# Kernel tuning notes

Hardware: AMD Instinct MI355X
Metric: run time of the kernel (lower is better)

The kernel has to match this reference:

```python
import jax, jax.numpy as jnp
import numpy as np

HEADS = 8
DIM_HEAD = 32


def setup_inputs() -> dict:
    key = jax.random.key(0)
    k1, k2, k3, k4 = jax.random.split(key, 4)
    dim, hidden = 256, HEADS * DIM_HEAD
    x = jax.random.normal(k1, (4, dim, 48, 48), dtype=jnp.float32)
    # 1x1 conv weights stored as [out_ch, in_ch]
    w_qkv = jax.random.normal(k2, (3 * hidden, dim), dtype=jnp.float32) * (dim ** -0.5)
    w_out = jax.random.normal(k3, (dim, hidden), dtype=jnp.float32) * (hidden ** -0.5)
    b_out = jax.random.normal(k4, (dim,), dtype=jnp.float32) * 0.01
    return {"x": x, "w_qkv": w_qkv, "w_out": w_out, "b_out": b_out}


def reference(x, w_qkv, w_out, b_out):
    B, C, H, W = x.shape
    n = H * W
    scale = DIM_HEAD ** -0.5
    # 1x1 conv QKV projection: [B, 3*hidden, H, W] -> [B, 3, heads, dh, n]
    qkv = jnp.einsum('oc,bchw->bohw', w_qkv, x).reshape(B, 3, HEADS, DIM_HEAD, n)
    q, k, v = qkv[:, 0], qkv[:, 1], qkv[:, 2]  # each [B, h, dh, n]
    sim = jnp.einsum('bhdi,bhdj->bhij', q, k) * scale  # [B, h, n, n]
    attn = jax.nn.softmax(sim, axis=-1)
    out = jnp.einsum('bhij,bhdj->bhdi', attn, v)  # [B, h, dh, n] -> channels (h d)
    out = out.reshape(B, HEADS * DIM_HEAD, H, W)
    return jnp.einsum('oc,bchw->bohw', w_out, out) + b_out[None, :, None, None]
```

## Files before the change

### kernel.cpp

```cpp
#include <hip/hip_runtime.h>
#include <hip/hip_bf16.h>

#define NSP 2304
#define NB  4

typedef unsigned short u16;
typedef __attribute__((ext_vector_type(8))) short short8;
typedef __attribute__((ext_vector_type(4))) short short4v;
typedef __attribute__((ext_vector_type(4))) float f32x4;
typedef __attribute__((ext_vector_type(4))) unsigned short u16x4;

#define K1S 0.25508040852656425f

static __device__ inline u16 f2bf(float f) {
  return __builtin_bit_cast(unsigned short, __float2bfloat16(f));
}

__global__ __launch_bounds__(256) void convert_w(
    const float* __restrict__ wq, const float* __restrict__ wo,
    u16* __restrict__ dst) {
  int i = (blockIdx.x * 256 + threadIdx.x) * 4;
  float4 v;
  if (i < 196608) v = *(const float4*)(wq + i);
  else            v = *(const float4*)(wo + (i - 196608));
  u16x4 p = {f2bf(v.x), f2bf(v.y), f2bf(v.z), f2bf(v.w)};
  *(u16x4*)(dst + i) = p;
}

__global__ __launch_bounds__(256) void transpose_x(
    const float* __restrict__ x, u16* __restrict__ xT) {
  __shared__ float tile[32][33];
  const int t = threadIdx.x;
  const int n0 = blockIdx.x * 32, c0 = blockIdx.y * 32, b = blockIdx.z;
  const float* xb = x + ((size_t)b * 256 + c0) * NSP + n0;
#pragma unroll
  for (int e = t; e < 1024; e += 256) {
    int cc = e >> 5, nn = e & 31;
    tile[cc][nn] = xb[(size_t)cc * NSP + nn];
  }
  __syncthreads();
  u16* xTb = xT + ((size_t)b * NSP + n0) * 256 + c0;
#pragma unroll
  for (int e = t; e < 1024; e += 256) {
    int nn = e >> 5, cc = e & 31;
    xTb[(size_t)nn * 256 + cc] = f2bf(tile[cc][nn]);
  }
}

template <int EPI>
__global__ __launch_bounds__(256) void gemm_mfma(
    const u16* __restrict__ A, const u16* __restrict__ B,
    u16* __restrict__ qkT, u16* __restrict__ vbuf,
    float* __restrict__ outf, const float* __restrict__ bias, int N) {
  __shared__ u16 As[64][264];
  __shared__ u16 Bs[64][264];
  const int t = threadIdx.x, lane = t & 63, wid = t >> 6;
  const int lo = lane & 15, g = lane >> 4;
  const int wr = wid >> 1, wc = wid & 1;
  const int row0 = blockIdx.y * 64, col0 = blockIdx.x * 64, b = blockIdx.z;

  const int sr = t >> 2, c4 = t & 3;
  const u16* Arow = A + (size_t)(row0 + sr) * 256;
  const u16* Brow = B + ((size_t)b * N + col0 + sr) * 256;
#pragma unroll
  for (int i = 0; i < 8; ++i) {
    int col = (c4 + 4 * i) * 8;
    *(uint4*)&As[sr][col] = *(const uint4*)&Arow[col];
    *(uint4*)&Bs[sr][col] = *(const uint4*)&Brow[col];
  }
  __syncthreads();

  f32x4 acc[2][2];
#pragma unroll
  for (int i = 0; i < 2; ++i)
#pragma unroll
    for (int j = 0; j < 2; ++j) acc[i][j] = (f32x4){0, 0, 0, 0};

  const int ar0 = wr * 32 + lo, br0 = wc * 32 + lo;
#pragma unroll
  for (int kk = 0; kk < 8; ++kk) {
    int kc = kk * 32 + g * 8;
    short8 a0 = *(const short8*)&As[ar0][kc];
    short8 a1 = *(const short8*)&As[ar0 + 16][kc];
    short8 b0 = *(const short8*)&Bs[br0][kc];
    short8 b1 = *(const short8*)&Bs[br0 + 16][kc];
    acc[0][0] = __builtin_amdgcn_mfma_f32_16x16x32_bf16(a0, b0, acc[0][0], 0, 0, 0);
    acc[0][1] = __builtin_amdgcn_mfma_f32_16x16x32_bf16(a0, b1, acc[0][1], 0, 0, 0);
    acc[1][0] = __builtin_amdgcn_mfma_f32_16x16x32_bf16(a1, b0, acc[1][0], 0, 0, 0);
    acc[1][1] = __builtin_amdgcn_mfma_f32_16x16x32_bf16(a1, b1, acc[1][1], 0, 0, 0);
  }

  const float qs = (EPI == 0 && row0 < 256) ? K1S : 1.0f;
#pragma unroll
  for (int m2 = 0; m2 < 2; ++m2)
#pragma unroll
    for (int n2 = 0; n2 < 2; ++n2) {
      int m = row0 + wr * 32 + m2 * 16 + g * 4;
      int n = col0 + wc * 32 + n2 * 16 + lo;
      if constexpr (EPI == 0) {
        if (row0 < 512) {
          u16x4 pk = {f2bf(acc[m2][n2][0] * qs), f2bf(acc[m2][n2][1] * qs),
                      f2bf(acc[m2][n2][2] * qs), f2bf(acc[m2][n2][3] * qs)};
          *(u16x4*)(qkT + ((size_t)b * NSP + n) * 512 + m) = pk;
        } else {
#pragma unroll
          for (int r = 0; r < 4; ++r)
            vbuf[((size_t)b * 256 + (m - 512 + r)) * NSP + n] =
                f2bf(acc[m2][n2][r]);
        }
      } else {
#pragma unroll
        for (int r = 0; r < 4; ++r)
          outf[((size_t)b * 256 + m + r) * NSP + n] =
              acc[m2][n2][r] + bias[m + r];
      }
    }
}

__global__ __launch_bounds__(256) void attn_mfma(
    const u16* __restrict__ qkT, const u16* __restrict__ vbuf,
    u16* __restrict__ attnoT) {
  const int it = blockIdx.x, h = blockIdx.y, b = blockIdx.z;
  const int t = threadIdx.x, lane = t & 63, wq = t >> 6;
  const int lo = lane & 15, g = lane >> 4;
  const int i0 = it * 64;

  const u16* qkTb = qkT + (size_t)b * NSP * 512;
  const u16* vb   = vbuf + ((size_t)b * 256 + h * 32) * NSP;
  u16* ob = attnoT + ((size_t)b * NSP + i0) * 256 + h * 32;

  __shared__ u16 Kt[2][64][40];
  __shared__ u16 Vs[2][32][72];

  short8 qf = *(const short8*)(qkTb + (size_t)(i0 + wq * 16 + lo) * 512 +
                               h * 32 + g * 8);

  const int kr = t >> 2, kp = (t & 3) * 8;
  const int vr = t >> 3, vp = (t & 7) * 8;
  const u16* ksrc = qkTb + 256 + h * 32 + kp;
  const u16* vsrc = vb + (size_t)vr * NSP + vp;

  uint4 kreg = *(const uint4*)(ksrc + (size_t)kr * 512);
  uint4 vreg = *(const uint4*)(vsrc);
  *(uint4*)&Kt[0][kr][kp] = kreg;
  *(uint4*)&Vs[0][vr][vp] = vreg;
  __syncthreads();

  short8 ones;
#pragma unroll
  for (int e = 0; e < 8; ++e) ones[e] = (short)0x3F80;

  f32x4 acc0 = {0, 0, 0, 0}, acc1 = {0, 0, 0, 0}, accl = {0, 0, 0, 0};

  for (int s = 0; s < 36; ++s) {
    const int cur = s & 1;
    if (s + 1 < 36) {
      int j0n = (s + 1) * 64;
      kreg = *(const uint4*)(ksrc + (size_t)(j0n + kr) * 512);
      vreg = *(const uint4*)(vsrc + j0n);
    }

    f32x4 sv[4];
#pragma unroll
    for (int jt = 0; jt < 4; ++jt) {
      short8 kf = *(const short8*)&Kt[cur][jt * 16 + lo][g * 8];
      sv[jt] = __builtin_amdgcn_mfma_f32_16x16x32_bf16(
          kf, qf, (f32x4){0, 0, 0, 0}, 0, 0, 0);
    }

    short8 pf0, pf1;
#pragma unroll
    for (int e = 0; e < 8; ++e) {
      pf0[e] = (short)f2bf(__builtin_amdgcn_exp2f(sv[e >> 2][e & 3]));
      pf1[e] = (short)f2bf(__builtin_amdgcn_exp2f(sv[2 + (e >> 2)][e & 3]));
    }

    short4v v00a = *(const short4v*)&Vs[cur][lo][4 * g];
    short4v v00b = *(const short4v*)&Vs[cur][lo][16 + 4 * g];
    short4v v01a = *(const short4v*)&Vs[cur][lo][32 + 4 * g];
    short4v v01b = *(const short4v*)&Vs[cur][lo][48 + 4 * g];
    short4v v10a = *(const short4v*)&Vs[cur][16 + lo][4 * g];
    short4v v10b = *(const short4v*)&Vs[cur][16 + lo][16 + 4 * g];
    short4v v11a = *(const short4v*)&Vs[cur][16 + lo][32 + 4 * g];
    short4v v11b = *(const short4v*)&Vs[cur][16 + lo][48 + 4 * g];
    short8 vf00 = __builtin_shufflevector(v00a, v00b, 0, 1, 2, 3, 4, 5, 6, 7);
    short8 vf01 = __builtin_shufflevector(v01a, v01b, 0, 1, 2, 3, 4, 5, 6, 7);
    short8 vf10 = __builtin_shufflevector(v10a, v10b, 0, 1, 2, 3, 4, 5, 6, 7);
    short8 vf11 = __builtin_shufflevector(v11a, v11b, 0, 1, 2, 3, 4, 5, 6, 7);

    acc0 = __builtin_amdgcn_mfma_f32_16x16x32_bf16(pf0, vf00, acc0, 0, 0, 0);
    acc1 = __builtin_amdgcn_mfma_f32_16x16x32_bf16(pf0, vf10, acc1, 0, 0, 0);
    accl = __builtin_amdgcn_mfma_f32_16x16x32_bf16(pf0, ones, accl, 0, 0, 0);
    acc0 = __builtin_amdgcn_mfma_f32_16x16x32_bf16(pf1, vf01, acc0, 0, 0, 0);
    acc1 = __builtin_amdgcn_mfma_f32_16x16x32_bf16(pf1, vf11, acc1, 0, 0, 0);
    accl = __builtin_amdgcn_mfma_f32_16x16x32_bf16(pf1, ones, accl, 0, 0, 0);

    if (s + 1 < 36) {
      *(uint4*)&Kt[cur ^ 1][kr][kp] = kreg;
      *(uint4*)&Vs[cur ^ 1][vr][vp] = vreg;
    }
    __syncthreads();
  }

#pragma unroll
  for (int r = 0; r < 4; ++r) {
    float inv = 1.0f / accl[r];
    int row = wq * 16 + g * 4 + r;
    ob[(size_t)row * 256 + lo]      = f2bf(acc0[r] * inv);
    ob[(size_t)row * 256 + 16 + lo] = f2bf(acc1[r] * inv);
  }
}

extern "C" void kernel_launch(void* const* d_in, const int* in_sizes, int n_in,
                              void* d_out, int out_size, void* d_ws, size_t ws_size,
                              hipStream_t stream) {
  const float* x     = (const float*)d_in[0];
  const float* w_qkv = (const float*)d_in[1];
  const float* w_out = (const float*)d_in[2];
  const float* b_out = (const float*)d_in[3];
  float* out = (float*)d_out;

  u16* wbf    = (u16*)d_ws;
  u16* xT     = wbf + 262144;
  u16* qkT    = xT + (size_t)NB * NSP * 256;
  u16* vbuf   = qkT + (size_t)NB * NSP * 512;
  u16* attnoT = vbuf + (size_t)NB * 256 * NSP;

  dim3 blk(256);
  convert_w<<<256, blk, 0, stream>>>(w_qkv, w_out, wbf);
  transpose_x<<<dim3(NSP / 32, 8, NB), blk, 0, stream>>>(x, xT);
  gemm_mfma<0><<<dim3(NSP / 64, 12, NB), blk, 0, stream>>>(
      wbf, xT, qkT, vbuf, nullptr, nullptr, NSP);
  attn_mfma<<<dim3(NSP / 64, 8, NB), blk, 0, stream>>>(qkT, vbuf, attnoT);
  gemm_mfma<1><<<dim3(NSP / 64, 4, NB), blk, 0, stream>>>(
      wbf + 196608, attnoT, nullptr, nullptr, out, b_out, NSP);
}
```

Before: 81.51 us.

## Give each attention wave two query tiles and pack bf16 conversions

The attention kernel now runs 128 threads per block instead of 256, and each wave handles 32 query rows instead of 16. Each K and V fragment read from LDS is therefore reused for two query tiles, halving LDS traffic per MFMA. Each thread issues twice the global loads when staging K and V, and the V shared tile padding changes from 72 to 68. The exp results are packed to bf16 with the v_cvt_pk_bf16_f32 instruction, trading fewer waves per block and more registers for better data reuse.

```diff
diff --git a/kernel.cpp b/kernel.cpp
--- a/kernel.cpp
+++ b/kernel.cpp
@@ -14,6 +14,11 @@
 
 static __device__ inline u16 f2bf(float f) {
   return __builtin_bit_cast(unsigned short, __float2bfloat16(f));
+}
+static __device__ inline unsigned cvtpk(float a, float b) {
+  unsigned r;
+  asm("v_cvt_pk_bf16_f32 %0, %1, %2" : "=v"(r) : "v"(a), "v"(b));
+  return r;
 }
 
 __global__ __launch_bounds__(256) void convert_w(
@@ -117,11 +122,11 @@
     }
 }
 
-__global__ __launch_bounds__(256) void attn_mfma(
+__global__ __launch_bounds__(128) void attn_mfma(
     const u16* __restrict__ qkT, const u16* __restrict__ vbuf,
     u16* __restrict__ attnoT) {
   const int it = blockIdx.x, h = blockIdx.y, b = blockIdx.z;
-  const int t = threadIdx.x, lane = t & 63, wq = t >> 6;
+  const int t = threadIdx.x, lane = t & 63, w = t >> 6;
   const int lo = lane & 15, g = lane >> 4;
   const int i0 = it * 64;
 
@@ -130,51 +135,50 @@
   u16* ob = attnoT + ((size_t)b * NSP + i0) * 256 + h * 32;
 
   __shared__ u16 Kt[2][64][40];
-  __shared__ u16 Vs[2][32][72];
-
-  short8 qf = *(const short8*)(qkTb + (size_t)(i0 + wq * 16 + lo) * 512 +
-                               h * 32 + g * 8);
+  __shared__ u16 Vs[2][32][68];
+
+  short8 qfA = *(const short8*)(qkTb + (size_t)(i0 + w * 32 + lo) * 512 +
+                                h * 32 + g * 8);
+  short8 qfB = *(const short8*)(qkTb + (size_t)(i0 + w * 32 + 16 + lo) * 512 +
+                                h * 32 + g * 8);
 
   const int kr = t >> 2, kp = (t & 3) * 8;
   const int vr = t >> 3, vp = (t & 7) * 8;
-  const u16* ksrc = qkTb + 256 + h * 32 + kp;
-  const u16* vsrc = vb + (size_t)vr * NSP + vp;
-
-  uint4 kreg = *(const uint4*)(ksrc + (size_t)kr * 512);
-  uint4 vreg = *(const uint4*)(vsrc);
-  *(uint4*)&Kt[0][kr][kp] = kreg;
-  *(uint4*)&Vs[0][vr][vp] = vreg;
+  const u16* ksrc  = qkTb + 256 + h * 32 + kp;
+  const u16* vsrc0 = vb + (size_t)vr * NSP + vp;
+  const u16* vsrc1 = vb + (size_t)(vr + 16) * NSP + vp;
+
+  uint4 k0 = *(const uint4*)(ksrc + (size_t)kr * 512);
+  uint4 k1 = *(const uint4*)(ksrc + (size_t)(kr + 32) * 512);
+  uint4 v0 = *(const uint4*)(vsrc0);
+  uint4 v1 = *(const uint4*)(vsrc1);
+  *(uint4*)&Kt[0][kr][kp]      = k0;
+  *(uint4*)&Kt[0][kr + 32][kp] = k1;
+  *(uint4*)&Vs[0][vr][vp]      = v0;
+  *(uint4*)&Vs[0][vr + 16][vp] = v1;
   __syncthreads();
 
   short8 ones;
 #pragma unroll
   for (int e = 0; e < 8; ++e) ones[e] = (short)0x3F80;
 
-  f32x4 acc0 = {0, 0, 0, 0}, acc1 = {0, 0, 0, 0}, accl = {0, 0, 0, 0};
+  f32x4 a0A = {0, 0, 0, 0}, a1A = {0, 0, 0, 0}, alA = {0, 0, 0, 0};
+  f32x4 a0B = {0, 0, 0, 0}, a1B = {0, 0, 0, 0}, alB = {0, 0, 0, 0};
 
   for (int s = 0; s < 36; ++s) {
     const int cur = s & 1;
     if (s + 1 < 36) {
       int j0n = (s + 1) * 64;
-      kreg = *(const uint4*)(ksrc + (size_t)(j0n + kr) * 512);
-      vreg = *(const uint4*)(vsrc + j0n);
-    }
-
-    f32x4 sv[4];
-#pragma unroll
-    for (int jt = 0; jt < 4; ++jt) {
-      short8 kf = *(const short8*)&Kt[cur][jt * 16 + lo][g * 8];
-      sv[jt] = __builtin_amdgcn_mfma_f32_16x16x32_bf16(
-          kf, qf, (f32x4){0, 0, 0, 0}, 0, 0, 0);
-    }
-
-    short8 pf0, pf1;
-#pragma unroll
-    for (int e = 0; e < 8; ++e) {
-      pf0[e] = (short)f2bf(__builtin_amdgcn_exp2f(sv[e >> 2][e & 3]));
-      pf1[e] = (short)f2bf(__builtin_amdgcn_exp2f(sv[2 + (e >> 2)][e & 3]));
-    }
-
+      k0 = *(const uint4*)(ksrc + (size_t)(j0n + kr) * 512);
+      k1 = *(const uint4*)(ksrc + (size_t)(j0n + kr + 32) * 512);
+      v0 = *(const uint4*)(vsrc0 + j0n);
+      v1 = *(const uint4*)(vsrc1 + j0n);
+    }
+
+    short8 kf0 = *(const short8*)&Kt[cur][lo][g * 8];
+    short8 kf1 = *(const short8*)&Kt[cur][16 + lo][g * 8];
+    short8 kf2 = *(const short8*)&Kt[cur][32 + lo][g * 8];
+    short8 kf3 = *(const short8*)&Kt[cur][48 + lo][g * 8];
     short4v v00a = *(const short4v*)&Vs[cur][lo][4 * g];
     short4v v00b = *(const short4v*)&Vs[cur][lo][16 + 4 * g];
     short4v v01a = *(const short4v*)&Vs[cur][lo][32 + 4 * g];
@@ -188,26 +192,61 @@
     short8 vf10 = __builtin_shufflevector(v10a, v10b, 0, 1, 2, 3, 4, 5, 6, 7);
     short8 vf11 = __builtin_shufflevector(v11a, v11b, 0, 1, 2, 3, 4, 5, 6, 7);
 
-    acc0 = __builtin_amdgcn_mfma_f32_16x16x32_bf16(pf0, vf00, acc0, 0, 0, 0);
-    acc1 = __builtin_amdgcn_mfma_f32_16x16x32_bf16(pf0, vf10, acc1, 0, 0, 0);
-    accl = __builtin_amdgcn_mfma_f32_16x16x32_bf16(pf0, ones, accl, 0, 0, 0);
-    acc0 = __builtin_amdgcn_mfma_f32_16x16x32_bf16(pf1, vf01, acc0, 0, 0, 0);
-    acc1 = __builtin_amdgcn_mfma_f32_16x16x32_bf16(pf1, vf11, acc1, 0, 0, 0);
-    accl = __builtin_amdgcn_mfma_f32_16x16x32_bf16(pf1, ones, accl, 0, 0, 0);
+#pragma unroll
+    for (int qh = 0; qh < 2; ++qh) {
+      short8 qf = qh ? qfB : qfA;
+      f32x4 sv0 = __builtin_amdgcn_mfma_f32_16x16x32_bf16(kf0, qf, (f32x4){0,0,0,0}, 0, 0, 0);
+      f32x4 sv1 = __builtin_amdgcn_mfma_f32_16x16x32_bf16(kf1, qf, (f32x4){0,0,0,0}, 0, 0, 0);
+      f32x4 sv2 = __builtin_amdgcn_mfma_f32_16x16x32_bf16(kf2, qf, (f32x4){0,0,0,0}, 0, 0, 0);
+      f32x4 sv3 = __builtin_amdgcn_mfma_f32_16x16x32_bf16(kf3, qf, (f32x4){0,0,0,0}, 0, 0, 0);
+
+      f32x4 e0, e1, e2, e3;
+#pragma unroll
+      for (int r = 0; r < 4; ++r) {
+        e0[r] = __builtin_amdgcn_exp2f(sv0[r]);
+        e1[r] = __builtin_amdgcn_exp2f(sv1[r]);
+        e2[r] = __builtin_amdgcn_exp2f(sv2[r]);
+        e3[r] = __builtin_amdgcn_exp2f(sv3[r]);
+      }
+      uint4 P0 = {cvtpk(e0[0], e0[1]), cvtpk(e0[2], e0[3]),
+                  cvtpk(e1[0], e1[1]), cvtpk(e1[2], e1[3])};
+      uint4 P1 = {cvtpk(e2[0], e2[1]), cvtpk(e2[2], e2[3]),
+                  cvtpk(e3[0], e3[1]), cvtpk(e3[2], e3[3])};
+      short8 pf0 = __builtin_bit_cast(short8, P0);
+      short8 pf1 = __builtin_bit_cast(short8, P1);
+
+      f32x4& c0 = qh ? a0B : a0A;
+      f32x4& c1 = qh ? a1B : a1A;
+      f32x4& cl = qh ? alB : alA;
+      c0 = __builtin_amdgcn_mfma_f32_16x16x32_bf16(pf0, vf00, c0, 0, 0, 0);
+      c1 = __builtin_amdgcn_mfma_f32_16x16x32_bf16(pf0, vf10, c1, 0, 0, 0);
+      cl = __builtin_amdgcn_mfma_f32_16x16x32_bf16(pf0, ones, cl, 0, 0, 0);
+      c0 = __builtin_amdgcn_mfma_f32_16x16x32_bf16(pf1, vf01, c0, 0, 0, 0);
+      c1 = __builtin_amdgcn_mfma_f32_16x16x32_bf16(pf1, vf11, c1, 0, 0, 0);
+      cl = __builtin_amdgcn_mfma_f32_16x16x32_bf16(pf1, ones, cl, 0, 0, 0);
+    }
 
     if (s + 1 < 36) {
-      *(uint4*)&Kt[cur ^ 1][kr][kp] = kreg;
-      *(uint4*)&Vs[cur ^ 1][vr][vp] = vreg;
+      *(uint4*)&Kt[cur ^ 1][kr][kp]      = k0;
+      *(uint4*)&Kt[cur ^ 1][kr + 32][kp] = k1;
+      *(uint4*)&Vs[cur ^ 1][vr][vp]      = v0;
+      *(uint4*)&Vs[cur ^ 1][vr + 16][vp] = v1;
     }
     __syncthreads();
   }
 
 #pragma unroll
-  for (int r = 0; r < 4; ++r) {
-    float inv = 1.0f / accl[r];
-    int row = wq * 16 + g * 4 + r;
-    ob[(size_t)row * 256 + lo]      = f2bf(acc0[r] * inv);
-    ob[(size_t)row * 256 + 16 + lo] = f2bf(acc1[r] * inv);
+  for (int qh = 0; qh < 2; ++qh) {
+    f32x4 c0 = qh ? a0B : a0A;
+    f32x4 c1 = qh ? a1B : a1A;
+    f32x4 cl = qh ? alB : alA;
+#pragma unroll
+    for (int r = 0; r < 4; ++r) {
+      float inv = 1.0f / cl[r];
+      int row = w * 32 + qh * 16 + g * 4 + r;
+      ob[(size_t)row * 256 + lo]      = f2bf(c0[r] * inv);
+      ob[(size_t)row * 256 + 16 + lo] = f2bf(c1[r] * inv);
+    }
   }
 }
 
@@ -231,7 +270,7 @@
   transpose_x<<<dim3(NSP / 32, 8, NB), blk, 0, stream>>>(x, xT);
   gemm_mfma<0><<<dim3(NSP / 64, 12, NB), blk, 0, stream>>>(
       wbf, xT, qkT, vbuf, nullptr, nullptr, NSP);
-  attn_mfma<<<dim3(NSP / 64, 8, NB), blk, 0, stream>>>(qkT, vbuf, attnoT);
+  attn_mfma<<<dim3(NSP / 64, 8, NB), dim3(128), 0, stream>>>(qkT, vbuf, attnoT);
   gemm_mfma<1><<<dim3(NSP / 64, 4, NB), blk, 0, stream>>>(
       wbf + 196608, attnoT, nullptr, nullptr, out, b_out, NSP);
 }
```

After: 81.50 us. Within noise of the previous version (-0.0%).
